# Kernel optimization log

Measured on AMD Instinct MI355X. Metric: run time of the kernel, lower is better.

## Reference

```python
import jax, jax.numpy as jnp
import numpy as np

NUM_HEADS = 12
DIM = 768
HEAD_DIM = DIM // NUM_HEADS


def setup_inputs() -> dict:
    key = jax.random.key(0)
    k1, k2, k3, k4 = jax.random.split(key, 4)
    B, N, C = 4, 8192, DIM
    x = jax.random.normal(k1, (B, N, C), dtype=jnp.float32)
    # torch nn.Linear stores weight as (out_features, in_features)
    W_qkv = jax.random.normal(k2, (3 * C, C), dtype=jnp.float32) * (1.0 / np.sqrt(C))
    W_proj = jax.random.normal(k3, (C, C), dtype=jnp.float32) * (1.0 / np.sqrt(C))
    b_proj = jax.random.normal(k4, (C,), dtype=jnp.float32) * 0.01
    return {"x": x, "W_qkv": W_qkv, "W_proj": W_proj, "b_proj": b_proj}


def reference(x, W_qkv, W_proj, b_proj):
    B, N, C = x.shape
    H, D = NUM_HEADS, HEAD_DIM
    qkv = x @ W_qkv.T                                  # [B,N,3C]
    qkv = qkv.reshape(B, N, 3, H, D).transpose(2, 0, 3, 1, 4)  # [3,B,H,N,D]
    q, k, v = qkv[0], qkv[1], qkv[2]
    q = jax.nn.elu(q) + 1.0
    k = jax.nn.elu(k) + 1.0
    k_sum = k.sum(axis=-2)                             # [B,H,D]
    kv = jnp.einsum('bhnd,bhne->bhde', k, v)           # [B,H,D,D]
    numerator = jnp.einsum('bhnd,bhde->bhne', q, kv)   # [B,H,N,D]
    denominator = jnp.einsum('bhnd,bhd->bhn', q, k_sum)
    out = numerator / (denominator[..., None] + 1e-6)
    out = out.transpose(0, 2, 1, 3).reshape(B, N, C)   # [B,N,C]
    out = out @ W_proj.T + b_proj
    return out
```

## Files before the change

### kernel.cpp

```cpp
#include <hip/hip_runtime.h>
#include <hip/hip_bf16.h>
#include <stdint.h>

typedef __attribute__((ext_vector_type(8))) short short8;
typedef __attribute__((ext_vector_type(4))) float floatx4;

#define NB 4
#define NN 8192
#define NC 768
#define NH 12
#define ND 64
#define LDQKV 2304

__device__ __forceinline__ float bf2f(ushort u) {
    union { float f; uint32_t i; } x; x.i = ((uint32_t)u) << 16; return x.f;
}
__device__ __forceinline__ ushort f2bf(float f) {
    union { float f; uint32_t i; } x; x.f = f;
    uint32_t r = x.i + 0x7fff + ((x.i >> 16) & 1);
    return (ushort)(r >> 16);
}
typedef const __attribute__((address_space(1))) uint32_t* gas1_t;
typedef __attribute__((address_space(3))) uint32_t* las3_t;
__device__ __forceinline__ void gl_lds16(const void* g, const void* l) {
    __builtin_amdgcn_global_load_lds((gas1_t)(uintptr_t)g,
                                     (las3_t)(uint32_t)(uintptr_t)l, 16, 0, 0);
}

__global__ __launch_bounds__(256) void cvt_bf16(const float* __restrict__ src,
                                                ushort* __restrict__ dst, int n) {
    const int i = (blockIdx.x * 256 + threadIdx.x) * 8;
    if (i >= n) return;
    const float4 a = *(const float4*)(src + i);
    const float4 b = *(const float4*)(src + i + 4);
    short8 v;
    v[0] = (short)f2bf(a.x); v[1] = (short)f2bf(a.y);
    v[2] = (short)f2bf(a.z); v[3] = (short)f2bf(a.w);
    v[4] = (short)f2bf(b.x); v[5] = (short)f2bf(b.y);
    v[6] = (short)f2bf(b.z); v[7] = (short)f2bf(b.w);
    *(short8*)(dst + i) = v;
}

template<int LDC, bool ELU, bool BIAS, typename OutT>
__global__ __launch_bounds__(256) void gemm_bt(const ushort* __restrict__ A,
                                               const ushort* __restrict__ Bw,
                                               const float* __restrict__ bias,
                                               OutT* __restrict__ Cout, int K) {
    __shared__ ushort As[128 * 32];
    __shared__ ushort Bs[128 * 32];
    const int t = threadIdx.x;
    const int w = t >> 6, lane = t & 63, l16 = lane & 15, quad = lane >> 4;
    const int wm = w & 1, wn = w >> 1;
    const int m0 = blockIdx.y * 128, n0 = blockIdx.x * 128;

    floatx4 acc[4][4] = {};

    const int rowA = t >> 2, chA = t & 3;
    const ushort* gA = A  + (size_t)(m0 + rowA) * K + chA * 8;
    const ushort* gB = Bw + (size_t)(n0 + rowA) * K + chA * 8;

    for (int k0 = 0; k0 < K; k0 += 32) {
        gl_lds16(gA + k0,                As + w * 512);
        gl_lds16(gA + k0 + 64 * K,       As + 2048 + w * 512);
        gl_lds16(gB + k0,                Bs + w * 512);
        gl_lds16(gB + k0 + 64 * K,       Bs + 2048 + w * 512);
        __syncthreads();
        short8 af[4], bfr[4];
        #pragma unroll
        for (int i = 0; i < 4; i++)
            af[i] = *(const short8*)&As[(wm * 64 + i * 16 + l16) * 32 + quad * 8];
        #pragma unroll
        for (int j = 0; j < 4; j++)
            bfr[j] = *(const short8*)&Bs[(wn * 64 + j * 16 + l16) * 32 + quad * 8];
        #pragma unroll
        for (int i = 0; i < 4; i++)
            #pragma unroll
            for (int j = 0; j < 4; j++)
                acc[i][j] = __builtin_amdgcn_mfma_f32_16x16x32_bf16(af[i], bfr[j], acc[i][j], 0, 0, 0);
        __syncthreads();
    }

    #pragma unroll
    for (int i = 0; i < 4; i++) {
        const int row = m0 + wm * 64 + i * 16 + quad * 4;
        #pragma unroll
        for (int j = 0; j < 4; j++) {
            const int col = n0 + wn * 64 + j * 16 + l16;
            float bval = 0.f;
            if (BIAS) bval = bias[col];
            #pragma unroll
            for (int r = 0; r < 4; r++) {
                float v = acc[i][j][r];
                if (ELU) { if (col < 2 * NC) v = (v > 0.f) ? v + 1.f : __expf(v); }
                if (BIAS) v += bval;
                if (sizeof(OutT) == 2) Cout[(size_t)(row + r) * LDC + col] = (OutT)f2bf(v);
                else                   Cout[(size_t)(row + r) * LDC + col] = (OutT)v;
            }
        }
    }
}

__global__ __launch_bounds__(256) void kv_ksum(const ushort* __restrict__ qkv,
                                               float* __restrict__ kvws,
                                               float* __restrict__ ksws) {
    __shared__ ushort klds[128 * 64];
    __shared__ ushort vlds[128 * 64];
    __shared__ float  kvred[64 * 64];
    __shared__ float  ksred[4][64];
    const int bh = blockIdx.y, b = bh / NH, h = bh % NH;
    const int t = threadIdx.x, w = t >> 6, lane = t & 63, l16 = lane & 15, quad = lane >> 4;
    const int n0 = blockIdx.x * 1024;
    const ushort* kbase = qkv + (size_t)(b * NN) * LDQKV + NC     + h * ND;
    const ushort* vbase = qkv + (size_t)(b * NN) * LDQKV + 2 * NC + h * ND;

    floatx4 acc[4][4] = {};
    float ksp = 0.f;
    const int rowT = t >> 3, ch = t & 7;

    for (int s = 0; s < 8; s++) {
        const int nb = n0 + s * 128;
        #pragma unroll
        for (int i = 0; i < 4; i++) {
            const size_t r = (size_t)(nb + i * 32 + rowT) * LDQKV + ch * 8;
            gl_lds16(kbase + r, klds + i * 2048 + w * 512);
            gl_lds16(vbase + r, vlds + i * 2048 + w * 512);
        }
        __syncthreads();
        short8 af[4], bfr[4];
        #pragma unroll
        for (int dt = 0; dt < 4; dt++) {
            short8 v;
            #pragma unroll
            for (int j = 0; j < 8; j++)
                v[j] = (short)klds[(w * 32 + quad * 8 + j) * 64 + dt * 16 + l16];
            af[dt] = v;
        }
        #pragma unroll
        for (int et = 0; et < 4; et++) {
            short8 v;
            #pragma unroll
            for (int j = 0; j < 8; j++)
                v[j] = (short)vlds[(w * 32 + quad * 8 + j) * 64 + et * 16 + l16];
            bfr[et] = v;
        }
        #pragma unroll
        for (int dt = 0; dt < 4; dt++)
            #pragma unroll
            for (int et = 0; et < 4; et++)
                acc[dt][et] = __builtin_amdgcn_mfma_f32_16x16x32_bf16(af[dt], bfr[et], acc[dt][et], 0, 0, 0);
        #pragma unroll
        for (int n = 0; n < 32; n++) ksp += bf2f(klds[(w * 32 + n) * 64 + lane]);
        __syncthreads();
    }

    if (w == 0) {
        #pragma unroll
        for (int dt = 0; dt < 4; dt++)
            #pragma unroll
            for (int et = 0; et < 4; et++)
                #pragma unroll
                for (int r = 0; r < 4; r++)
                    kvred[(dt * 16 + quad * 4 + r) * 64 + et * 16 + l16] = acc[dt][et][r];
    }
    ksred[w][lane] = ksp;
    __syncthreads();
    if (w != 0) {
        #pragma unroll
        for (int dt = 0; dt < 4; dt++)
            #pragma unroll
            for (int et = 0; et < 4; et++)
                #pragma unroll
                for (int r = 0; r < 4; r++)
                    atomicAdd(&kvred[(dt * 16 + quad * 4 + r) * 64 + et * 16 + l16], acc[dt][et][r]);
    }
    __syncthreads();
    for (int i = t; i < 4096; i += 256) atomicAdd(&kvws[(size_t)bh * 4096 + i], kvred[i]);
    if (t < 64) atomicAdd(&ksws[bh * 64 + t], ksred[0][t] + ksred[1][t] + ksred[2][t] + ksred[3][t]);
}

__global__ __launch_bounds__(256) void attn_apply(const ushort* __restrict__ qkv,
                                                  const float* __restrict__ kvws,
                                                  const float* __restrict__ ksws,
                                                  ushort* __restrict__ outpre) {
    __shared__ ushort kvb[64 * 80];
    const int bh = blockIdx.y, b = bh / NH, h = bh % NH;
    const int t = threadIdx.x, w = t >> 6, lane = t & 63, l16 = lane & 15, quad = lane >> 4;

    for (int i = t; i < 4096; i += 256) {
        const int d = i >> 6, e = i & 63;
        kvb[d * 80 + e] = f2bf(kvws[(size_t)bh * 4096 + i]);
    }
    for (int i = t; i < 1024; i += 256) {
        const int d = i >> 4, c = i & 15;
        kvb[d * 80 + 64 + c] = (c == 0) ? f2bf(ksws[bh * 64 + d]) : (ushort)0;
    }
    __syncthreads();

    short8 bfr[5][2];
    #pragma unroll
    for (int et = 0; et < 5; et++)
        #pragma unroll
        for (int ks = 0; ks < 2; ks++) {
            short8 v;
            #pragma unroll
            for (int j = 0; j < 8; j++)
                v[j] = (short)kvb[(ks * 32 + quad * 8 + j) * 80 + et * 16 + l16];
            bfr[et][ks] = v;
        }

    const ushort* qbase = qkv + (size_t)(b * NN) * LDQKV + h * ND;
    ushort* obase = outpre + (size_t)(b * NN) * NC + h * ND;
    const int n0 = blockIdx.x * 1024;

    for (int it = 0; it < 16; it++) {
        const int nt = n0 + (it * 4 + w) * 16;
        const ushort* qp = qbase + (size_t)(nt + l16) * LDQKV + quad * 8;
        const short8 a0 = *(const short8*)qp;
        const short8 a1 = *(const short8*)(qp + 32);
        floatx4 acc[5] = {};
        #pragma unroll
        for (int et = 0; et < 5; et++) {
            acc[et] = __builtin_amdgcn_mfma_f32_16x16x32_bf16(a0, bfr[et][0], acc[et], 0, 0, 0);
            acc[et] = __builtin_amdgcn_mfma_f32_16x16x32_bf16(a1, bfr[et][1], acc[et], 0, 0, 0);
        }
        float dv[4];
        #pragma unroll
        for (int r = 0; r < 4; r++) dv[r] = __shfl(acc[4][r], lane & 48);
        #pragma unroll
        for (int et = 0; et < 4; et++)
            #pragma unroll
            for (int r = 0; r < 4; r++) {
                const float o = acc[et][r] / (dv[r] + 1e-6f);
                obase[(size_t)(nt + quad * 4 + r) * NC + et * 16 + l16] = f2bf(o);
            }
    }
}

__global__ void zero_f32(float* p, int n) {
    const int i = blockIdx.x * 256 + threadIdx.x;
    if (i < n) p[i] = 0.f;
}

extern "C" void kernel_launch(void* const* d_in, const int* in_sizes, int n_in,
                              void* d_out, int out_size, void* d_ws, size_t ws_size,
                              hipStream_t stream) {
    (void)in_sizes; (void)n_in; (void)out_size; (void)ws_size;
    const float* X     = (const float*)d_in[0];
    const float* Wqkv  = (const float*)d_in[1];
    const float* Wproj = (const float*)d_in[2];
    const float* bproj = (const float*)d_in[3];
    float* out = (float*)d_out;

    char* ws = (char*)d_ws;
    size_t off = 0;
    ushort* qkv     = (ushort*)(ws + off); off += (size_t)32768 * 2304 * 2;
    ushort* outpre  = (ushort*)(ws + off); off += (size_t)32768 * 768 * 2;
    ushort* xbf     = (ushort*)(ws + off); off += (size_t)32768 * 768 * 2;
    ushort* wqkvbf  = (ushort*)(ws + off); off += (size_t)2304 * 768 * 2;
    ushort* wprojbf = (ushort*)(ws + off); off += (size_t)768 * 768 * 2;
    float*  kvws    = (float*)(ws + off);  off += (size_t)48 * 4096 * 4;
    float*  ksws    = (float*)(ws + off);

    const int nx = 32768 * 768, nwq = 2304 * 768, nwp = 768 * 768;
    cvt_bf16<<<nx  / (256 * 8), 256, 0, stream>>>(X,     xbf,     nx);
    cvt_bf16<<<nwq / (256 * 8), 256, 0, stream>>>(Wqkv,  wqkvbf,  nwq);
    cvt_bf16<<<nwp / (256 * 8), 256, 0, stream>>>(Wproj, wprojbf, nwp);

    const int nzero = 48 * 4096 + 48 * 64;
    zero_f32<<<(nzero + 255) / 256, 256, 0, stream>>>(kvws, nzero);

    gemm_bt<LDQKV, true, false, ushort><<<dim3(18, 256), 256, 0, stream>>>(xbf, wqkvbf, nullptr, qkv, NC);
    kv_ksum<<<dim3(8, 48), 256, 0, stream>>>(qkv, kvws, ksws);
    attn_apply<<<dim3(8, 48), 256, 0, stream>>>(qkv, kvws, ksws, outpre);
    gemm_bt<NC, false, true, float><<<dim3(6, 256), 256, 0, stream>>>(outpre, wprojbf, bproj, out, NC);
}
```

Baseline: 498.2 us.

## Fuse conversions, widen GEMM K-step, split KV reduction deterministically, compute ksum via MFMA

Result: slower. 515.0 us (+3.4%).

```diff
diff --git a/kernel.cpp b/kernel.cpp
--- a/kernel.cpp
+++ b/kernel.cpp
@@ -11,6 +11,7 @@
 #define NH 12
 #define ND 64
 #define LDQKV 2304
+#define NSPLIT 16
 
 __device__ __forceinline__ float bf2f(ushort u) {
     union { float f; uint32_t i; } x; x.i = ((uint32_t)u) << 16; return x.f;
@@ -27,18 +28,26 @@
                                      (las3_t)(uint32_t)(uintptr_t)l, 16, 0, 0);
 }
 
-__global__ __launch_bounds__(256) void cvt_bf16(const float* __restrict__ src,
-                                                ushort* __restrict__ dst, int n) {
-    const int i = (blockIdx.x * 256 + threadIdx.x) * 8;
-    if (i >= n) return;
-    const float4 a = *(const float4*)(src + i);
-    const float4 b = *(const float4*)(src + i + 4);
+__global__ __launch_bounds__(256) void cvt_all(const float* __restrict__ X,
+                                               const float* __restrict__ Wq,
+                                               const float* __restrict__ Wp,
+                                               ushort* __restrict__ xbf,
+                                               ushort* __restrict__ wqbf,
+                                               ushort* __restrict__ wpbf) {
+    const int nx = 32768 * 768, nwq = 2304 * 768, nwp = 768 * 768;
+    int i = (blockIdx.x * 256 + threadIdx.x) * 8;
+    const float* src; ushort* dst;
+    if (i < nx)            { src = X + i;              dst = xbf + i; }
+    else if (i < nx + nwq) { i -= nx;  src = Wq + i;   dst = wqbf + i; }
+    else                   { i -= nx + nwq; if (i >= nwp) return; src = Wp + i; dst = wpbf + i; }
+    const float4 a = *(const float4*)src;
+    const float4 b = *(const float4*)(src + 4);
     short8 v;
     v[0] = (short)f2bf(a.x); v[1] = (short)f2bf(a.y);
     v[2] = (short)f2bf(a.z); v[3] = (short)f2bf(a.w);
     v[4] = (short)f2bf(b.x); v[5] = (short)f2bf(b.y);
     v[6] = (short)f2bf(b.z); v[7] = (short)f2bf(b.w);
-    *(short8*)(dst + i) = v;
+    *(short8*)dst = v;
 }
 
 template<int LDC, bool ELU, bool BIAS, typename OutT>
@@ -46,8 +55,8 @@
                                                const ushort* __restrict__ Bw,
                                                const float* __restrict__ bias,
                                                OutT* __restrict__ Cout, int K) {
-    __shared__ ushort As[128 * 32];
-    __shared__ ushort Bs[128 * 32];
+    __shared__ ushort As[2][128 * 32];
+    __shared__ ushort Bs[2][128 * 32];
     const int t = threadIdx.x;
     const int w = t >> 6, lane = t & 63, l16 = lane & 15, quad = lane >> 4;
     const int wm = w & 1, wn = w >> 1;
@@ -59,24 +68,30 @@
     const ushort* gA = A  + (size_t)(m0 + rowA) * K + chA * 8;
     const ushort* gB = Bw + (size_t)(n0 + rowA) * K + chA * 8;
 
-    for (int k0 = 0; k0 < K; k0 += 32) {
-        gl_lds16(gA + k0,                As + w * 512);
-        gl_lds16(gA + k0 + 64 * K,       As + 2048 + w * 512);
-        gl_lds16(gB + k0,                Bs + w * 512);
-        gl_lds16(gB + k0 + 64 * K,       Bs + 2048 + w * 512);
+    for (int k0 = 0; k0 < K; k0 += 64) {
+        #pragma unroll
+        for (int p = 0; p < 2; p++) {
+            gl_lds16(gA + k0 + p * 32,                &As[p][w * 512]);
+            gl_lds16(gA + k0 + p * 32 + 64 * (size_t)K, &As[p][2048 + w * 512]);
+            gl_lds16(gB + k0 + p * 32,                &Bs[p][w * 512]);
+            gl_lds16(gB + k0 + p * 32 + 64 * (size_t)K, &Bs[p][2048 + w * 512]);
+        }
         __syncthreads();
-        short8 af[4], bfr[4];
-        #pragma unroll
-        for (int i = 0; i < 4; i++)
-            af[i] = *(const short8*)&As[(wm * 64 + i * 16 + l16) * 32 + quad * 8];
-        #pragma unroll
-        for (int j = 0; j < 4; j++)
-            bfr[j] = *(const short8*)&Bs[(wn * 64 + j * 16 + l16) * 32 + quad * 8];
-        #pragma unroll
-        for (int i = 0; i < 4; i++)
+        #pragma unroll
+        for (int p = 0; p < 2; p++) {
+            short8 af[4], bfr[4];
+            #pragma unroll
+            for (int i = 0; i < 4; i++)
+                af[i] = *(const short8*)&As[p][(wm * 64 + i * 16 + l16) * 32 + quad * 8];
             #pragma unroll
             for (int j = 0; j < 4; j++)
-                acc[i][j] = __builtin_amdgcn_mfma_f32_16x16x32_bf16(af[i], bfr[j], acc[i][j], 0, 0, 0);
+                bfr[j] = *(const short8*)&Bs[p][(wn * 64 + j * 16 + l16) * 32 + quad * 8];
+            #pragma unroll
+            for (int i = 0; i < 4; i++)
+                #pragma unroll
+                for (int j = 0; j < 4; j++)
+                    acc[i][j] = __builtin_amdgcn_mfma_f32_16x16x32_bf16(af[i], bfr[j], acc[i][j], 0, 0, 0);
+        }
         __syncthreads();
     }
 
@@ -88,36 +103,42 @@
             const int col = n0 + wn * 64 + j * 16 + l16;
             float bval = 0.f;
             if (BIAS) bval = bias[col];
+            OutT* cp = Cout + (size_t)row * LDC + col;
             #pragma unroll
             for (int r = 0; r < 4; r++) {
                 float v = acc[i][j][r];
                 if (ELU) { if (col < 2 * NC) v = (v > 0.f) ? v + 1.f : __expf(v); }
                 if (BIAS) v += bval;
-                if (sizeof(OutT) == 2) Cout[(size_t)(row + r) * LDC + col] = (OutT)f2bf(v);
-                else                   Cout[(size_t)(row + r) * LDC + col] = (OutT)v;
+                if (sizeof(OutT) == 2) *cp = (OutT)f2bf(v);
+                else                   *cp = (OutT)v;
+                cp += LDC;
             }
         }
     }
 }
 
 __global__ __launch_bounds__(256) void kv_ksum(const ushort* __restrict__ qkv,
-                                               float* __restrict__ kvws,
-                                               float* __restrict__ ksws) {
+                                               float* __restrict__ kvpart,
+                                               float* __restrict__ kspart) {
     __shared__ ushort klds[128 * 64];
     __shared__ ushort vlds[128 * 64];
     __shared__ float  kvred[64 * 64];
     __shared__ float  ksred[4][64];
     const int bh = blockIdx.y, b = bh / NH, h = bh % NH;
     const int t = threadIdx.x, w = t >> 6, lane = t & 63, l16 = lane & 15, quad = lane >> 4;
-    const int n0 = blockIdx.x * 1024;
+    const int n0 = blockIdx.x * (NN * NB / NSPLIT / 4);
     const ushort* kbase = qkv + (size_t)(b * NN) * LDQKV + NC     + h * ND;
     const ushort* vbase = qkv + (size_t)(b * NN) * LDQKV + 2 * NC + h * ND;
 
     floatx4 acc[4][4] = {};
-    float ksp = 0.f;
+    floatx4 acc5[4] = {};
+    short8 ones;
+    #pragma unroll
+    for (int j = 0; j < 8; j++) ones[j] = (l16 == 0) ? (short)0x3F80 : (short)0;
+
     const int rowT = t >> 3, ch = t & 7;
 
-    for (int s = 0; s < 8; s++) {
+    for (int s = 0; s < 4; s++) {
         const int nb = n0 + s * 128;
         #pragma unroll
         for (int i = 0; i < 4; i++) {
@@ -144,12 +165,12 @@
             bfr[et] = v;
         }
         #pragma unroll
-        for (int dt = 0; dt < 4; dt++)
+        for (int dt = 0; dt < 4; dt++) {
             #pragma unroll
             for (int et = 0; et < 4; et++)
                 acc[dt][et] = __builtin_amdgcn_mfma_f32_16x16x32_bf16(af[dt], bfr[et], acc[dt][et], 0, 0, 0);
-        #pragma unroll
-        for (int n = 0; n < 32; n++) ksp += bf2f(klds[(w * 32 + n) * 64 + lane]);
+            acc5[dt] = __builtin_amdgcn_mfma_f32_16x16x32_bf16(af[dt], ones, acc5[dt], 0, 0, 0);
+        }
         __syncthreads();
     }
 
@@ -162,7 +183,13 @@
                 for (int r = 0; r < 4; r++)
                     kvred[(dt * 16 + quad * 4 + r) * 64 + et * 16 + l16] = acc[dt][et][r];
     }
-    ksred[w][lane] = ksp;
+    if (l16 == 0) {
+        #pragma unroll
+        for (int dt = 0; dt < 4; dt++)
+            #pragma unroll
+            for (int r = 0; r < 4; r++)
+                ksred[w][dt * 16 + quad * 4 + r] = acc5[dt][r];
+    }
     __syncthreads();
     if (w != 0) {
         #pragma unroll
@@ -174,13 +201,34 @@
                     atomicAdd(&kvred[(dt * 16 + quad * 4 + r) * 64 + et * 16 + l16], acc[dt][et][r]);
     }
     __syncthreads();
-    for (int i = t; i < 4096; i += 256) atomicAdd(&kvws[(size_t)bh * 4096 + i], kvred[i]);
-    if (t < 64) atomicAdd(&ksws[bh * 64 + t], ksred[0][t] + ksred[1][t] + ksred[2][t] + ksred[3][t]);
+    float* kvp = kvpart + ((size_t)blockIdx.x * 48 + bh) * 4096;
+    for (int i = t; i < 4096; i += 256) kvp[i] = kvred[i];
+    if (t < 64) kspart[((size_t)blockIdx.x * 48 + bh) * 64 + t] =
+        ksred[0][t] + ksred[1][t] + ksred[2][t] + ksred[3][t];
+}
+
+__global__ __launch_bounds__(256) void reduce_kvks(const float* __restrict__ kvpart,
+                                                   const float* __restrict__ kspart,
+                                                   float* __restrict__ kvfinal,
+                                                   float* __restrict__ ksfinal) {
+    const int bh = blockIdx.y, t = threadIdx.x;
+    if (blockIdx.x < 16) {
+        const int i = blockIdx.x * 256 + t;
+        float s = 0.f;
+        #pragma unroll
+        for (int p = 0; p < NSPLIT; p++) s += kvpart[((size_t)p * 48 + bh) * 4096 + i];
+        kvfinal[(size_t)bh * 4096 + i] = s;
+    } else if (t < 64) {
+        float s = 0.f;
+        #pragma unroll
+        for (int p = 0; p < NSPLIT; p++) s += kspart[((size_t)p * 48 + bh) * 64 + t];
+        ksfinal[bh * 64 + t] = s;
+    }
 }
 
 __global__ __launch_bounds__(256) void attn_apply(const ushort* __restrict__ qkv,
-                                                  const float* __restrict__ kvws,
-                                                  const float* __restrict__ ksws,
+                                                  const float* __restrict__ kvfinal,
+                                                  const float* __restrict__ ksfinal,
                                                   ushort* __restrict__ outpre) {
     __shared__ ushort kvb[64 * 80];
     const int bh = blockIdx.y, b = bh / NH, h = bh % NH;
@@ -188,11 +236,11 @@
 
     for (int i = t; i < 4096; i += 256) {
         const int d = i >> 6, e = i & 63;
-        kvb[d * 80 + e] = f2bf(kvws[(size_t)bh * 4096 + i]);
+        kvb[d * 80 + e] = f2bf(kvfinal[(size_t)bh * 4096 + i]);
     }
     for (int i = t; i < 1024; i += 256) {
         const int d = i >> 4, c = i & 15;
-        kvb[d * 80 + 64 + c] = (c == 0) ? f2bf(ksws[bh * 64 + d]) : (ushort)0;
+        kvb[d * 80 + 64 + c] = (c == 0) ? f2bf(ksfinal[bh * 64 + d]) : (ushort)0;
     }
     __syncthreads();
 
@@ -210,9 +258,9 @@
 
     const ushort* qbase = qkv + (size_t)(b * NN) * LDQKV + h * ND;
     ushort* obase = outpre + (size_t)(b * NN) * NC + h * ND;
-    const int n0 = blockIdx.x * 1024;
-
-    for (int it = 0; it < 16; it++) {
+    const int n0 = blockIdx.x * (NN * NB / NSPLIT / 4);
+
+    for (int it = 0; it < 8; it++) {
         const int nt = n0 + (it * 4 + w) * 16;
         const ushort* qp = qbase + (size_t)(nt + l16) * LDQKV + quad * 8;
         const short8 a0 = *(const short8*)qp;
@@ -234,11 +282,6 @@
                 obase[(size_t)(nt + quad * 4 + r) * NC + et * 16 + l16] = f2bf(o);
             }
     }
-}
-
-__global__ void zero_f32(float* p, int n) {
-    const int i = blockIdx.x * 256 + threadIdx.x;
-    if (i < n) p[i] = 0.f;
 }
 
 extern "C" void kernel_launch(void* const* d_in, const int* in_sizes, int n_in,
@@ -258,19 +301,17 @@
     ushort* xbf     = (ushort*)(ws + off); off += (size_t)32768 * 768 * 2;
     ushort* wqkvbf  = (ushort*)(ws + off); off += (size_t)2304 * 768 * 2;
     ushort* wprojbf = (ushort*)(ws + off); off += (size_t)768 * 768 * 2;
-    float*  kvws    = (float*)(ws + off);  off += (size_t)48 * 4096 * 4;
-    float*  ksws    = (float*)(ws + off);
-
-    const int nx = 32768 * 768, nwq = 2304 * 768, nwp = 768 * 768;
-    cvt_bf16<<<nx  / (256 * 8), 256, 0, stream>>>(X,     xbf,     nx);
-    cvt_bf16<<<nwq / (256 * 8), 256, 0, stream>>>(Wqkv,  wqkvbf,  nwq);
-    cvt_bf16<<<nwp / (256 * 8), 256, 0, stream>>>(Wproj, wprojbf, nwp);
-
-    const int nzero = 48 * 4096 + 48 * 64;
-    zero_f32<<<(nzero + 255) / 256, 256, 0, stream>>>(kvws, nzero);
+    float* kvpart  = (float*)xbf;
+    float* kspart  = kvpart + (size_t)NSPLIT * 48 * 4096;
+    float* kvfinal = kspart + (size_t)NSPLIT * 48 * 64;
+    float* ksfinal = kvfinal + (size_t)48 * 4096;
+
+    const int ncvt = (32768 * 768 + 2304 * 768 + 768 * 768) / 8 / 256;
+    cvt_all<<<ncvt, 256, 0, stream>>>(X, Wqkv, Wproj, xbf, wqkvbf, wprojbf);
 
     gemm_bt<LDQKV, true, false, ushort><<<dim3(18, 256), 256, 0, stream>>>(xbf, wqkvbf, nullptr, qkv, NC);
-    kv_ksum<<<dim3(8, 48), 256, 0, stream>>>(qkv, kvws, ksws);
-    attn_apply<<<dim3(8, 48), 256, 0, stream>>>(qkv, kvws, ksws, outpre);
+    kv_ksum<<<dim3(NSPLIT, 48), 256, 0, stream>>>(qkv, kvpart, kspart);
+    reduce_kvks<<<dim3(17, 48), 256, 0, stream>>>(kvpart, kspart, kvfinal, ksfinal);
+    attn_apply<<<dim3(NSPLIT, 48), 256, 0, stream>>>(qkv, kvfinal, ksfinal, outpre);
     gemm_bt<NC, false, true, float><<<dim3(6, 256), 256, 0, stream>>>(outpre, wprojbf, bproj, out, NC);
 }
```
